# Kernel optimization log

Hardware: AMD Instinct MI355X
Metric: run time of the kernel (lower is better)

## Reference

```python
import jax, jax.numpy as jnp
import numpy as np

N = 100000   # nodes
E = 300000   # edges
D = 256      # emb_dim
L = 5        # num_layers
SELF_LOOP_BOND_TYPE = 4
BN_EPS = 1e-5


def setup_inputs() -> dict:
    key = jax.random.key(0)
    ks = jax.random.split(key, 12)
    s = 0.05
    x = jax.random.randint(ks[0], (N, 2), 0, 3)
    edge_index = jax.random.randint(ks[1], (2, E), 0, N)
    edge_attr = jax.random.randint(ks[2], (E, 2), 0, 3)
    x_emb1 = jax.random.normal(ks[3], (120, D), dtype=jnp.float32) * s
    x_emb2 = jax.random.normal(ks[4], (3, D), dtype=jnp.float32) * s
    edge_emb1 = jax.random.normal(ks[5], (L, 6, D), dtype=jnp.float32) * s
    edge_emb2 = jax.random.normal(ks[6], (L, 3, D), dtype=jnp.float32) * s
    W1 = jax.random.normal(ks[7], (L, D, 2 * D), dtype=jnp.float32) * (1.0 / np.sqrt(D))
    b1 = jnp.zeros((L, 2 * D), dtype=jnp.float32)
    W2 = jax.random.normal(ks[8], (L, 2 * D, D), dtype=jnp.float32) * (1.0 / np.sqrt(2 * D))
    b2 = jnp.zeros((L, D), dtype=jnp.float32)
    bn_gamma = jnp.ones((L - 1, D), dtype=jnp.float32)
    bn_beta = jnp.zeros((L - 1, D), dtype=jnp.float32)
    return dict(x=x, edge_index=edge_index, edge_attr=edge_attr,
                x_emb1=x_emb1, x_emb2=x_emb2,
                edge_emb1=edge_emb1, edge_emb2=edge_emb2,
                W1=W1, b1=b1, W2=W2, b2=b2,
                bn_gamma=bn_gamma, bn_beta=bn_beta)


def reference(x, edge_index, edge_attr, x_emb1, x_emb2, edge_emb1, edge_emb2,
              W1, b1, W2, b2, bn_gamma, bn_beta):
    n = x.shape[0]
    loop = jnp.arange(n)
    # add_self_loops: append (i, i) for every node
    src = jnp.concatenate([edge_index[0], loop])  # [E+N]
    dst = jnp.concatenate([edge_index[1], loop])  # [E+N]
    # self-loop edge_attr = (bond_type=4, direction=0)
    self_attr = jnp.concatenate([
        jnp.full((n, 1), SELF_LOOP_BOND_TYPE, dtype=edge_attr.dtype),
        jnp.zeros((n, 1), dtype=edge_attr.dtype)], axis=1)
    ea = jnp.concatenate([edge_attr, self_attr], axis=0)  # [E+N, 2]

    out = x_emb1[x[:, 0]] + x_emb2[x[:, 1]]  # [N, D]
    for l in range(L):
        e_emb = edge_emb1[l][ea[:, 0]] + edge_emb2[l][ea[:, 1]]  # [E+N, D]
        msg = out[src] + e_emb                                   # gather + message
        agg = jax.ops.segment_sum(msg, dst, num_segments=n)      # scatter-add
        h = jax.nn.relu(agg @ W1[l] + b1[l]) @ W2[l] + b2[l]     # GIN MLP
        if l < L - 1:
            mean = h.mean(axis=0)
            var = h.var(axis=0)  # biased var, matches torch BN training
            h = (h - mean) * jax.lax.rsqrt(var + BN_EPS) * bn_gamma[l] + bn_beta[l]
            h = jax.nn.relu(h)
        out = h
    return out
```

## Files before the change

kernel.cpp:

```cpp
#include <hip/hip_runtime.h>

typedef unsigned short u16;
typedef unsigned int u32;

#define DD 256

typedef short  s16x8 __attribute__((ext_vector_type(8)));
typedef short  s16x4 __attribute__((ext_vector_type(4)));
typedef float  f32x4 __attribute__((ext_vector_type(4)));

__device__ __forceinline__ float b2f(u16 u){
  union { u32 i; float f; } c; c.i = ((u32)u) << 16; return c.f;
}
__device__ __forceinline__ u16 f2b(float f){
  union { float f; u32 i; } c; c.f = f;
  u32 b = c.i + 0x7FFFu + ((c.i >> 16) & 1u);
  return (u16)(b >> 16);
}

__global__ void NodeEncoder_72971494359603_kernel(){}

__global__ void probe_dtype(const u32* w, u32* flag){
  if (threadIdx.x == 0 && blockIdx.x == 0){
    int cnt = 0;
    for (int i = 0; i < 256; i++){
      u32 low = w[i] & 0xFFFFu;
      u32 e = (low >> 7) & 0xFFu;
      if (e >= 0x60u && e <= 0x7Eu) cnt++;
    }
    *flag = (cnt >= 192) ? 1u : 0u;
  }
}

__global__ void cvt_in(const void* src, u16* dst, int n, const u32* flag){
  int i = blockIdx.x * 256 + threadIdx.x;
  if (i < n){
    if (*flag){
      dst[i] = ((const u16*)src)[i];
    } else {
      dst[i] = f2b(((const float*)src)[i]);
    }
  }
}

__global__ void store_out(const u16* h, void* dout, int n, const u32* flag){
  int i = blockIdx.x * 256 + threadIdx.x;
  if (i < n){
    if (*flag){
      ((u16*)dout)[i] = h[i];
    } else {
      ((float*)dout)[i] = b2f(h[i]);
    }
  }
}

__global__ void zero_int(int* p, int n){
  int i = blockIdx.x * 256 + threadIdx.x;
  if (i < n) p[i] = 0;
}

__global__ void build_table(const u16* ee1, const u16* ee2, float* TBL){
  int b = blockIdx.x;
  int l = b / 18, c = b % 18, a = c / 3, bb = c % 3;
  int j = threadIdx.x;
  TBL[b * DD + j] = b2f(ee1[(l * 6 + a) * DD + j]) + b2f(ee2[(l * 3 + bb) * DD + j]);
}

__global__ void hist_kernel(const int* dst, int* counts, int E){
  int e = blockIdx.x * 256 + threadIdx.x;
  if (e < E) atomicAdd(&counts[dst[e]], 1);
}

__global__ void scan_sums(const int* counts, int* bsum, int N){
  __shared__ int red[256];
  int tid = threadIdx.x;
  int base = blockIdx.x * 1024;
  int s = 0;
  for (int i = tid; i < 1024; i += 256){
    int g = base + i;
    if (g < N) s += counts[g];
  }
  red[tid] = s;
  __syncthreads();
  for (int off = 128; off > 0; off >>= 1){
    if (tid < off) red[tid] += red[tid + off];
    __syncthreads();
  }
  if (tid == 0) bsum[blockIdx.x] = red[0];
}

__global__ void scan_top(int* bsum, int nb){
  if (threadIdx.x == 0 && blockIdx.x == 0){
    int acc = 0;
    for (int i = 0; i < nb; i++){ int t = bsum[i]; bsum[i] = acc; acc += t; }
  }
}

__global__ void scan_block(const int* counts, const int* bsum,
                           int* offsets, int* cursor, int N){
  __shared__ int tsum[256];
  int b = blockIdx.x;
  int tid = threadIdx.x;
  int base = b * 1024;
  int v0, v1, v2, v3;
  int g = base + tid * 4;
  v0 = (g + 0 < N) ? counts[g + 0] : 0;
  v1 = (g + 1 < N) ? counts[g + 1] : 0;
  v2 = (g + 2 < N) ? counts[g + 2] : 0;
  v3 = (g + 3 < N) ? counts[g + 3] : 0;
  tsum[tid] = v0 + v1 + v2 + v3;
  __syncthreads();
  for (int off = 1; off < 256; off <<= 1){
    int t = (tid >= off) ? tsum[tid - off] : 0;
    __syncthreads();
    tsum[tid] += t;
    __syncthreads();
  }
  int excl = (tid == 0 ? 0 : tsum[tid - 1]) + bsum[b];
  if (g + 0 < N){ offsets[g + 0] = excl; cursor[g + 0] = excl; } excl += v0;
  if (g + 1 < N){ offsets[g + 1] = excl; cursor[g + 1] = excl; } excl += v1;
  if (g + 2 < N){ offsets[g + 2] = excl; cursor[g + 2] = excl; } excl += v2;
  if (g + 3 < N){ offsets[g + 3] = excl; cursor[g + 3] = excl; }
}

__global__ void fill_csr(const int* ei, const int* ea, int* cursor,
                         int* payload, int E){
  int e = blockIdx.x * 256 + threadIdx.x;
  if (e < E){
    int d = ei[E + e];
    int pos = atomicAdd(&cursor[d], 1);
    int a = ea[2 * e], bb = ea[2 * e + 1];
    payload[pos] = ei[e] | ((a * 3 + bb) << 17);
  }
}

__global__ void node_embed(const int* x, const u16* xe1, const u16* xe2,
                           u16* out, int N){
  int idx = blockIdx.x * 256 + threadIdx.x;
  if (idx < N * DD){
    int n = idx >> 8, j = idx & 255;
    int x0 = x[2 * n], x1 = x[2 * n + 1];
    out[idx] = f2b(b2f(xe1[x0 * DD + j]) + b2f(xe2[x1 * DD + j]));
  }
}

__global__ void aggregate(const u16* __restrict__ feat, const float* __restrict__ TBL,
                          const int* __restrict__ offsets, const int* __restrict__ counts,
                          const int* __restrict__ payload, u16* __restrict__ agg, int N,
                          const float* __restrict__ sums, const u16* __restrict__ gamma,
                          const u16* __restrict__ beta, float invN, int apply_bn){
  __shared__ __align__(16) float T[18 * DD];
  int tid = threadIdx.x;
  for (int i = tid; i < 18 * DD; i += 256) T[i] = TBL[i];
  __syncthreads();
  int wave = tid >> 6, lane = tid & 63;
  int c4 = lane * 4;
  float sc[4], sh[4];
  if (apply_bn){
#pragma unroll
    for (int e = 0; e < 4; e++){
      int j = c4 + e;
      float mean = sums[j] * invN;
      float var = sums[DD + j] * invN - mean * mean;
      if (var < 0.f) var = 0.f;
      float scl = rsqrtf(var + 1e-5f) * b2f(gamma[j]);
      sc[e] = scl; sh[e] = b2f(beta[j]) - mean * scl;
    }
  } else {
#pragma unroll
    for (int e = 0; e < 4; e++){ sc[e] = 1.f; sh[e] = 0.f; }
  }
  int n0 = blockIdx.x * 32 + wave * 8;
  for (int u = 0; u < 8; u++){
    int n = n0 + u;
    if (n >= N) return;
    s16x4 sv = *(const s16x4*)(feat + (size_t)n * DD + c4);
    f32x4 tb = *(const f32x4*)(T + 12 * DD + c4);
    float v0 = b2f((u16)sv[0]) * sc[0] + sh[0];
    float v1 = b2f((u16)sv[1]) * sc[1] + sh[1];
    float v2 = b2f((u16)sv[2]) * sc[2] + sh[2];
    float v3 = b2f((u16)sv[3]) * sc[3] + sh[3];
    if (apply_bn){
      v0 = fmaxf(v0, 0.f); v1 = fmaxf(v1, 0.f);
      v2 = fmaxf(v2, 0.f); v3 = fmaxf(v3, 0.f);
    }
    float a0 = v0 + tb[0], a1 = v1 + tb[1], a2 = v2 + tb[2], a3 = v3 + tb[3];
    int e0 = offsets[n], cnt = counts[n];
    for (int e = e0; e < e0 + cnt; e++){
      int pl = payload[e];
      int src = pl & 0x1FFFF;
      int idx = pl >> 17;
      s16x4 rv = *(const s16x4*)(feat + (size_t)src * DD + c4);
      f32x4 tv = *(const f32x4*)(T + idx * DD + c4);
      float w0 = b2f((u16)rv[0]) * sc[0] + sh[0];
      float w1 = b2f((u16)rv[1]) * sc[1] + sh[1];
      float w2 = b2f((u16)rv[2]) * sc[2] + sh[2];
      float w3 = b2f((u16)rv[3]) * sc[3] + sh[3];
      if (apply_bn){
        w0 = fmaxf(w0, 0.f); w1 = fmaxf(w1, 0.f);
        w2 = fmaxf(w2, 0.f); w3 = fmaxf(w3, 0.f);
      }
      a0 += w0 + tv[0];
      a1 += w1 + tv[1];
      a2 += w2 + tv[2];
      a3 += w3 + tv[3];
    }
    s16x4 o;
    o[0] = (short)f2b(a0); o[1] = (short)f2b(a1);
    o[2] = (short)f2b(a2); o[3] = (short)f2b(a3);
    *(s16x4*)(agg + (size_t)n * DD + c4) = o;
  }
}

__global__ void pack_B(const u16* __restrict__ W, u16* __restrict__ Wp, int K, int Nc){
  int idx = blockIdx.x * 256 + threadIdx.x;
  int lane = idx & 63;
  int t = idx >> 6;
  int nk = K >> 5;
  int ksub = t % nk, cblk = t / nk;
  if (cblk >= (Nc >> 4)) return;
  int col = cblk * 16 + (lane & 15);
  int krow = ksub * 32 + (lane >> 4) * 8;
  u16* dst = Wp + (size_t)idx * 8;
#pragma unroll
  for (int e = 0; e < 8; e++)
    dst[e] = W[(size_t)(krow + e) * Nc + col];
}

__global__ void mlp_fused(const u16* __restrict__ A, const u16* __restrict__ Wp1,
                          const u16* __restrict__ bias1, const u16* __restrict__ Wp2,
                          const u16* __restrict__ bias2, u16* __restrict__ H,
                          float* __restrict__ partial, int npart, int M){
  __shared__ __align__(16) u16 As[64 * 256];
  __shared__ __align__(16) u16 Ms[2][64 * 128];
  int tid = threadIdx.x, lane = tid & 63, wave = tid >> 6;
  int wr = wave >> 2, wc = wave & 3;
  int row0 = blockIdx.x * 64;
  int lr = lane & 15, hi = lane >> 4;

  int srow = tid >> 5, slot = tid & 31;
#pragma unroll
  for (int p = 0; p < 4; p++){
    int r = p * 16 + srow;
    int gr = row0 + r; if (gr > M - 1) gr = M - 1;
    s16x8 v = *(const s16x8*)(A + (size_t)gr * DD + slot * 8);
    *(s16x8*)((char*)As + r * 512 + ((slot * 16) ^ ((r & 7) << 4))) = v;
  }
  __syncthreads();

  f32x4 zero = {0.f, 0.f, 0.f, 0.f};
  f32x4 acc2[2][4];
#pragma unroll
  for (int m = 0; m < 2; m++)
#pragma unroll
    for (int n = 0; n < 4; n++) acc2[m][n] = zero;
  f32x4 acc1[2][2];

  auto G1 = [&](int cc){
#pragma unroll
    for (int m = 0; m < 2; m++)
#pragma unroll
      for (int n = 0; n < 2; n++) acc1[m][n] = zero;
#pragma unroll
    for (int ks = 0; ks < 8; ks++){
      s16x8 af[2];
#pragma unroll
      for (int m = 0; m < 2; m++){
        int arow = wr * 32 + m * 16 + lr;
        af[m] = *(const s16x8*)((const char*)As + arow * 512 +
                                ((ks * 64 + hi * 16) ^ ((arow & 7) << 4)));
      }
#pragma unroll
      for (int n = 0; n < 2; n++){
        int cb = cc * 8 + wc * 2 + n;
        s16x8 bf = *(const s16x8*)(Wp1 + (((size_t)cb * 8 + ks) * 64 + lane) * 8);
        acc1[0][n] = __builtin_amdgcn_mfma_f32_16x16x32_bf16(af[0], bf, acc1[0][n], 0, 0, 0);
        acc1[1][n] = __builtin_amdgcn_mfma_f32_16x16x32_bf16(af[1], bf, acc1[1][n], 0, 0, 0);
      }
    }
  };
  auto WMS = [&](int cc, int buf){
    char* ms = (char*)Ms[buf];
#pragma unroll
    for (int n = 0; n < 2; n++){
      float bv = b2f(bias1[cc * 128 + wc * 32 + n * 16 + lr]);
      int c2 = (wc * 32 + n * 16 + lr) * 2;
#pragma unroll
      for (int m = 0; m < 2; m++)
#pragma unroll
        for (int r = 0; r < 4; r++){
          int mrow = wr * 32 + m * 16 + hi * 4 + r;
          float v = fmaxf(acc1[m][n][r] + bv, 0.f);
          *(u16*)(ms + mrow * 256 + (c2 ^ ((mrow & 7) << 4))) = f2b(v);
        }
    }
  };

  G1(0);
  WMS(0, 0);
  __syncthreads();

#pragma unroll
  for (int c = 0; c < 4; c++){
    const char* ms = (const char*)Ms[c & 1];
#pragma unroll
    for (int ks = 0; ks < 4; ks++){
      s16x8 mf[2];
#pragma unroll
      for (int m = 0; m < 2; m++){
        int mrow = wr * 32 + m * 16 + lr;
        mf[m] = *(const s16x8*)(ms + mrow * 256 +
                                ((ks * 64 + hi * 16) ^ ((mrow & 7) << 4)));
      }
#pragma unroll
      for (int n = 0; n < 4; n++){
        int cb2 = wc * 4 + n;
        s16x8 wf = *(const s16x8*)(Wp2 + (((size_t)cb2 * 16 + c * 4 + ks) * 64 + lane) * 8);
        acc2[0][n] = __builtin_amdgcn_mfma_f32_16x16x32_bf16(mf[0], wf, acc2[0][n], 0, 0, 0);
        acc2[1][n] = __builtin_amdgcn_mfma_f32_16x16x32_bf16(mf[1], wf, acc2[1][n], 0, 0, 0);
      }
    }
    if (c < 3){
      G1(c + 1);
      WMS(c + 1, (c + 1) & 1);
      __syncthreads();
    }
  }

#pragma unroll
  for (int n = 0; n < 4; n++){
    float bv = b2f(bias2[wc * 64 + n * 16 + lr]);
    int c2 = (wc * 64 + n * 16 + lr) * 2;
#pragma unroll
    for (int m = 0; m < 2; m++)
#pragma unroll
      for (int r = 0; r < 4; r++){
        int mrow = wr * 32 + m * 16 + hi * 4 + r;
        *(u16*)((char*)As + mrow * 512 + (c2 ^ ((mrow & 7) << 4))) = f2b(acc2[m][n][r] + bv);
      }
  }
  __syncthreads();

  float s[8], q[8];
#pragma unroll
  for (int e = 0; e < 8; e++){ s[e] = 0.f; q[e] = 0.f; }
  int sl = tid & 31;
#pragma unroll
  for (int p = 0; p < 4; p++){
    int r = p * 16 + (tid >> 5);
    s16x8 v = *(const s16x8*)((const char*)As + r * 512 + ((sl << 4) ^ ((r & 7) << 4)));
    int gr = row0 + r;
    if (gr < M){
      *(s16x8*)(H + (size_t)gr * DD + sl * 8) = v;
      if (partial){
#pragma unroll
        for (int e = 0; e < 8; e++){
          float f = b2f((u16)v[e]);
          s[e] += f; q[e] += f * f;
        }
      }
    }
  }
  if (partial){
#pragma unroll
    for (int e = 0; e < 8; e++){
      s[e] += __shfl_xor(s[e], 32);
      q[e] += __shfl_xor(q[e], 32);
    }
    float* redS = (float*)Ms;
    float* redQ = redS + 8 * 256;
    if (lane < 32){
#pragma unroll
      for (int e = 0; e < 8; e++){
        redS[wave * 256 + sl * 8 + e] = s[e];
        redQ[wave * 256 + sl * 8 + e] = q[e];
      }
    }
    __syncthreads();
    if (tid < 256){
      float a = 0.f, b = 0.f;
#pragma unroll
      for (int w = 0; w < 8; w++){ a += redS[w * 256 + tid]; b += redQ[w * 256 + tid]; }
      partial[(size_t)blockIdx.x * DD + tid] = a;
      partial[(size_t)(npart + blockIdx.x) * DD + tid] = b;
    }
  }
}

__global__ void bn_reduce(const float* __restrict__ partial, float* __restrict__ sums,
                          int npart){
  int b = blockIdx.x, which = b >> 3, jg = b & 7;
  int t = threadIdx.x;
  int j = jg * 32 + (t >> 3);
  int li = t & 7;
  float s = 0.f;
  for (int i = li; i < npart; i += 8)
    s += partial[(size_t)(which * npart + i) * DD + j];
  s += __shfl_xor(s, 1); s += __shfl_xor(s, 2); s += __shfl_xor(s, 4);
  if (li == 0) sums[which * DD + j] = s;
}

extern "C" void kernel_launch(void* const* d_in, const int* in_sizes, int n_in,
                              void* d_out, int out_size, void* d_ws, size_t ws_size,
                              hipStream_t stream){
  (void)n_in; (void)out_size; (void)ws_size;
  const int* x    = (const int*)d_in[0];
  const int* ei   = (const int*)d_in[1];
  const int* ea   = (const int*)d_in[2];
  const void* xe1 = d_in[3];
  const void* xe2 = d_in[4];
  const void* ee1 = d_in[5];
  const void* ee2 = d_in[6];
  const void* W1  = d_in[7];
  const void* b1  = d_in[8];
  const void* W2  = d_in[9];
  const void* b2  = d_in[10];
  const void* gam = d_in[11];
  const void* bet = d_in[12];

  int N = in_sizes[0] / 2;
  int E = in_sizes[1] / 2;
  int NB = (N + 1023) / 1024;
  const int L = 5;
  int nblk = (N + 63) / 64;
  int npart = nblk;

  char* base = (char*)d_ws;
  size_t off = 0;
  u32* flag    = (u32*)(base + off);   off += 256;
  float* TBL   = (float*)(base + off); off += ((size_t)L * 18 * DD * 4 + 255) & ~(size_t)255;
  int* counts  = (int*)(base + off);   off += ((size_t)N * 4 + 255) & ~(size_t)255;
  int* offsets = (int*)(base + off);   off += ((size_t)N * 4 + 255) & ~(size_t)255;
  int* cursor  = (int*)(base + off);   off += ((size_t)N * 4 + 255) & ~(size_t)255;
  int* bsum    = (int*)(base + off);   off += ((size_t)NB * 4 + 255) & ~(size_t)255;
  int* payload = (int*)(base + off);   off += ((size_t)E * 4 + 255) & ~(size_t)255;
  float* part  = (float*)(base + off); off += ((size_t)2 * npart * DD * 4 + 255) & ~(size_t)255;
  float* sums  = (float*)(base + off); off += ((size_t)2 * DD * 4 + 255) & ~(size_t)255;
  u16* wx1  = (u16*)(base + off); off += ((size_t)120 * DD * 2 + 255) & ~(size_t)255;
  u16* wx2  = (u16*)(base + off); off += ((size_t)3 * DD * 2 + 255) & ~(size_t)255;
  u16* wee1 = (u16*)(base + off); off += ((size_t)L * 6 * DD * 2 + 255) & ~(size_t)255;
  u16* wee2 = (u16*)(base + off); off += ((size_t)L * 3 * DD * 2 + 255) & ~(size_t)255;
  u16* wW1  = (u16*)(base + off); off += ((size_t)L * DD * 2 * DD * 2 + 255) & ~(size_t)255;
  u16* wb1  = (u16*)(base + off); off += ((size_t)L * 2 * DD * 2 + 255) & ~(size_t)255;
  u16* wW2  = (u16*)(base + off); off += ((size_t)L * 2 * DD * DD * 2 + 255) & ~(size_t)255;
  u16* wb2  = (u16*)(base + off); off += ((size_t)L * DD * 2 + 255) & ~(size_t)255;
  u16* wgam = (u16*)(base + off); off += ((size_t)(L - 1) * DD * 2 + 255) & ~(size_t)255;
  u16* wbet = (u16*)(base + off); off += ((size_t)(L - 1) * DD * 2 + 255) & ~(size_t)255;
  u16* Wp1  = (u16*)(base + off); off += ((size_t)L * DD * 2 * DD * 2 + 255) & ~(size_t)255;
  u16* Wp2  = (u16*)(base + off); off += ((size_t)L * 2 * DD * DD * 2 + 255) & ~(size_t)255;
  u16* feat = (u16*)(base + off); off += ((size_t)N * DD * 2 + 255) & ~(size_t)255;
  u16* agg  = (u16*)(base + off); off += ((size_t)N * DD * 2 + 255) & ~(size_t)255;

  probe_dtype<<<1, 64, 0, stream>>>((const u32*)xe1, flag);
  cvt_in<<<(120 * DD + 255) / 256, 256, 0, stream>>>(xe1, wx1, 120 * DD, flag);
  cvt_in<<<(3 * DD + 255) / 256, 256, 0, stream>>>(xe2, wx2, 3 * DD, flag);
  cvt_in<<<(L * 6 * DD + 255) / 256, 256, 0, stream>>>(ee1, wee1, L * 6 * DD, flag);
  cvt_in<<<(L * 3 * DD + 255) / 256, 256, 0, stream>>>(ee2, wee2, L * 3 * DD, flag);
  cvt_in<<<(L * DD * 2 * DD + 255) / 256, 256, 0, stream>>>(W1, wW1, L * DD * 2 * DD, flag);
  cvt_in<<<(L * 2 * DD + 255) / 256, 256, 0, stream>>>(b1, wb1, L * 2 * DD, flag);
  cvt_in<<<(L * 2 * DD * DD + 255) / 256, 256, 0, stream>>>(W2, wW2, L * 2 * DD * DD, flag);
  cvt_in<<<(L * DD + 255) / 256, 256, 0, stream>>>(b2, wb2, L * DD, flag);
  cvt_in<<<((L - 1) * DD + 255) / 256, 256, 0, stream>>>(gam, wgam, (L - 1) * DD, flag);
  cvt_in<<<((L - 1) * DD + 255) / 256, 256, 0, stream>>>(bet, wbet, (L - 1) * DD, flag);

  build_table<<<90, 256, 0, stream>>>(wee1, wee2, TBL);
  for (int l = 0; l < L; l++){
    pack_B<<<64, 256, 0, stream>>>(wW1 + (size_t)l * DD * 2 * DD,
                                   Wp1 + (size_t)l * DD * 2 * DD, DD, 2 * DD);
    pack_B<<<64, 256, 0, stream>>>(wW2 + (size_t)l * 2 * DD * DD,
                                   Wp2 + (size_t)l * 2 * DD * DD, 2 * DD, DD);
  }
  zero_int<<<(N + 255) / 256, 256, 0, stream>>>(counts, N);
  hist_kernel<<<(E + 255) / 256, 256, 0, stream>>>(ei + E, counts, E);
  scan_sums<<<NB, 256, 0, stream>>>(counts, bsum, N);
  scan_top<<<1, 64, 0, stream>>>(bsum, NB);
  scan_block<<<NB, 256, 0, stream>>>(counts, bsum, offsets, cursor, N);
  fill_csr<<<(E + 255) / 256, 256, 0, stream>>>(ei, ea, cursor, payload, E);

  node_embed<<<(N * DD + 255) / 256, 256, 0, stream>>>(x, wx1, wx2, feat, N);

  float invN = 1.0f / (float)N;

  for (int l = 0; l < L; l++){
    aggregate<<<(N + 31) / 32, 256, 0, stream>>>(
        feat, TBL + (size_t)l * 18 * DD, offsets, counts, payload, agg, N,
        sums, wgam + (size_t)(l > 0 ? l - 1 : 0) * DD,
        wbet + (size_t)(l > 0 ? l - 1 : 0) * DD, invN, l > 0 ? 1 : 0);

    mlp_fused<<<nblk, 512, 0, stream>>>(
        agg, Wp1 + (size_t)l * DD * 2 * DD, wb1 + (size_t)l * 2 * DD,
        Wp2 + (size_t)l * 2 * DD * DD, wb2 + (size_t)l * DD, feat,
        (l < L - 1) ? part : (float*)nullptr, npart, N);

    if (l < L - 1){
      bn_reduce<<<16, 256, 0, stream>>>(part, sums, npart);
    }
  }

  store_out<<<(N * DD + 255) / 256, 256, 0, stream>>>(feat, d_out, N * DD, flag);
}
```

Baseline: 1.636 ms.

## Fuse neighbor aggregation into MLP kernel and ping-pong feature buffers

Merges the aggregate kernel into the fused MLP kernel: each 64-row block gathers neighbor features, applies the previous layer's BN and ReLU, adds edge embeddings from a table staged in the Ms shared buffer, and writes the aggregated rows straight into the swizzled As tile. The intermediate agg tensor's global write and read are dropped, and two feature buffers alternate between layers. The per-layer pack_B launches are also batched into one 2D launch per weight. In exchange, the irregular gather now runs inside a kernel with heavy shared-memory use and launch bounds, which may limit latency hiding for the gather phase.

Measured after the change: 1.646 ms. Within noise of the previous version (+0.6%).

```diff
diff --git a/kernel.cpp b/kernel.cpp
--- a/kernel.cpp
+++ b/kernel.cpp
@@ -144,75 +144,9 @@
   }
 }
 
-__global__ void aggregate(const u16* __restrict__ feat, const float* __restrict__ TBL,
-                          const int* __restrict__ offsets, const int* __restrict__ counts,
-                          const int* __restrict__ payload, u16* __restrict__ agg, int N,
-                          const float* __restrict__ sums, const u16* __restrict__ gamma,
-                          const u16* __restrict__ beta, float invN, int apply_bn){
-  __shared__ __align__(16) float T[18 * DD];
-  int tid = threadIdx.x;
-  for (int i = tid; i < 18 * DD; i += 256) T[i] = TBL[i];
-  __syncthreads();
-  int wave = tid >> 6, lane = tid & 63;
-  int c4 = lane * 4;
-  float sc[4], sh[4];
-  if (apply_bn){
-#pragma unroll
-    for (int e = 0; e < 4; e++){
-      int j = c4 + e;
-      float mean = sums[j] * invN;
-      float var = sums[DD + j] * invN - mean * mean;
-      if (var < 0.f) var = 0.f;
-      float scl = rsqrtf(var + 1e-5f) * b2f(gamma[j]);
-      sc[e] = scl; sh[e] = b2f(beta[j]) - mean * scl;
-    }
-  } else {
-#pragma unroll
-    for (int e = 0; e < 4; e++){ sc[e] = 1.f; sh[e] = 0.f; }
-  }
-  int n0 = blockIdx.x * 32 + wave * 8;
-  for (int u = 0; u < 8; u++){
-    int n = n0 + u;
-    if (n >= N) return;
-    s16x4 sv = *(const s16x4*)(feat + (size_t)n * DD + c4);
-    f32x4 tb = *(const f32x4*)(T + 12 * DD + c4);
-    float v0 = b2f((u16)sv[0]) * sc[0] + sh[0];
-    float v1 = b2f((u16)sv[1]) * sc[1] + sh[1];
-    float v2 = b2f((u16)sv[2]) * sc[2] + sh[2];
-    float v3 = b2f((u16)sv[3]) * sc[3] + sh[3];
-    if (apply_bn){
-      v0 = fmaxf(v0, 0.f); v1 = fmaxf(v1, 0.f);
-      v2 = fmaxf(v2, 0.f); v3 = fmaxf(v3, 0.f);
-    }
-    float a0 = v0 + tb[0], a1 = v1 + tb[1], a2 = v2 + tb[2], a3 = v3 + tb[3];
-    int e0 = offsets[n], cnt = counts[n];
-    for (int e = e0; e < e0 + cnt; e++){
-      int pl = payload[e];
-      int src = pl & 0x1FFFF;
-      int idx = pl >> 17;
-      s16x4 rv = *(const s16x4*)(feat + (size_t)src * DD + c4);
-      f32x4 tv = *(const f32x4*)(T + idx * DD + c4);
-      float w0 = b2f((u16)rv[0]) * sc[0] + sh[0];
-      float w1 = b2f((u16)rv[1]) * sc[1] + sh[1];
-      float w2 = b2f((u16)rv[2]) * sc[2] + sh[2];
-      float w3 = b2f((u16)rv[3]) * sc[3] + sh[3];
-      if (apply_bn){
-        w0 = fmaxf(w0, 0.f); w1 = fmaxf(w1, 0.f);
-        w2 = fmaxf(w2, 0.f); w3 = fmaxf(w3, 0.f);
-      }
-      a0 += w0 + tv[0];
-      a1 += w1 + tv[1];
-      a2 += w2 + tv[2];
-      a3 += w3 + tv[3];
-    }
-    s16x4 o;
-    o[0] = (short)f2b(a0); o[1] = (short)f2b(a1);
-    o[2] = (short)f2b(a2); o[3] = (short)f2b(a3);
-    *(s16x4*)(agg + (size_t)n * DD + c4) = o;
-  }
-}
-
-__global__ void pack_B(const u16* __restrict__ W, u16* __restrict__ Wp, int K, int Nc){
+__global__ void pack_B(const u16* __restrict__ W0, u16* __restrict__ Wp0, int K, int Nc){
+  const u16* W = W0 + (size_t)blockIdx.y * K * Nc;
+  u16* Wp = Wp0 + (size_t)blockIdx.y * K * Nc;
   int idx = blockIdx.x * 256 + threadIdx.x;
   int lane = idx & 63;
   int t = idx >> 6;
@@ -227,24 +161,83 @@
     dst[e] = W[(size_t)(krow + e) * Nc + col];
 }
 
-__global__ void mlp_fused(const u16* __restrict__ A, const u16* __restrict__ Wp1,
-                          const u16* __restrict__ bias1, const u16* __restrict__ Wp2,
-                          const u16* __restrict__ bias2, u16* __restrict__ H,
-                          float* __restrict__ partial, int npart, int M){
+__global__ __launch_bounds__(512, 4)
+void layer_fused(const u16* __restrict__ feat, const float* __restrict__ TBL,
+                 const int* __restrict__ offsets, const int* __restrict__ counts,
+                 const int* __restrict__ payload,
+                 const u16* __restrict__ Wp1, const u16* __restrict__ bias1,
+                 const u16* __restrict__ Wp2, const u16* __restrict__ bias2,
+                 u16* __restrict__ H, float* __restrict__ partial, int npart, int M,
+                 const float* __restrict__ sums, const u16* __restrict__ gamma,
+                 const u16* __restrict__ beta, float invN, int apply_bn){
   __shared__ __align__(16) u16 As[64 * 256];
   __shared__ __align__(16) u16 Ms[2][64 * 128];
+  float* T = (float*)Ms;
   int tid = threadIdx.x, lane = tid & 63, wave = tid >> 6;
   int wr = wave >> 2, wc = wave & 3;
   int row0 = blockIdx.x * 64;
   int lr = lane & 15, hi = lane >> 4;
 
-  int srow = tid >> 5, slot = tid & 31;
-#pragma unroll
-  for (int p = 0; p < 4; p++){
-    int r = p * 16 + srow;
-    int gr = row0 + r; if (gr > M - 1) gr = M - 1;
-    s16x8 v = *(const s16x8*)(A + (size_t)gr * DD + slot * 8);
-    *(s16x8*)((char*)As + r * 512 + ((slot * 16) ^ ((r & 7) << 4))) = v;
+  for (int i = tid; i < 18 * DD; i += 512) T[i] = TBL[i];
+  __syncthreads();
+
+  {
+    int c4 = lane * 4;
+    float sc[4], sh[4];
+    if (apply_bn){
+#pragma unroll
+      for (int e = 0; e < 4; e++){
+        int j = c4 + e;
+        float mean = sums[j] * invN;
+        float var = sums[DD + j] * invN - mean * mean;
+        if (var < 0.f) var = 0.f;
+        float scl = rsqrtf(var + 1e-5f) * b2f(gamma[j]);
+        sc[e] = scl; sh[e] = b2f(beta[j]) - mean * scl;
+      }
+    } else {
+#pragma unroll
+      for (int e = 0; e < 4; e++){ sc[e] = 1.f; sh[e] = 0.f; }
+    }
+    for (int u = 0; u < 8; u++){
+      int r = wave * 8 + u;
+      int n = row0 + r; if (n > M - 1) n = M - 1;
+      s16x4 sv = *(const s16x4*)(feat + (size_t)n * DD + c4);
+      f32x4 tb = *(const f32x4*)(T + 12 * DD + c4);
+      float v0 = b2f((u16)sv[0]) * sc[0] + sh[0];
+      float v1 = b2f((u16)sv[1]) * sc[1] + sh[1];
+      float v2 = b2f((u16)sv[2]) * sc[2] + sh[2];
+      float v3 = b2f((u16)sv[3]) * sc[3] + sh[3];
+      if (apply_bn){
+        v0 = fmaxf(v0, 0.f); v1 = fmaxf(v1, 0.f);
+        v2 = fmaxf(v2, 0.f); v3 = fmaxf(v3, 0.f);
+      }
+      float a0 = v0 + tb[0], a1 = v1 + tb[1], a2 = v2 + tb[2], a3 = v3 + tb[3];
+      int e0 = offsets[n], cnt = counts[n];
+      for (int e = e0; e < e0 + cnt; e++){
+        int pl = payload[e];
+        int src = pl & 0x1FFFF;
+        int idx = pl >> 17;
+        s16x4 rv = *(const s16x4*)(feat + (size_t)src * DD + c4);
+        f32x4 tv = *(const f32x4*)(T + idx * DD + c4);
+        float w0 = b2f((u16)rv[0]) * sc[0] + sh[0];
+        float w1 = b2f((u16)rv[1]) * sc[1] + sh[1];
+        float w2 = b2f((u16)rv[2]) * sc[2] + sh[2];
+        float w3 = b2f((u16)rv[3]) * sc[3] + sh[3];
+        if (apply_bn){
+          w0 = fmaxf(w0, 0.f); w1 = fmaxf(w1, 0.f);
+          w2 = fmaxf(w2, 0.f); w3 = fmaxf(w3, 0.f);
+        }
+        a0 += w0 + tv[0];
+        a1 += w1 + tv[1];
+        a2 += w2 + tv[2];
+        a3 += w3 + tv[3];
+      }
+      s16x4 o;
+      o[0] = (short)f2b(a0); o[1] = (short)f2b(a1);
+      o[2] = (short)f2b(a2); o[3] = (short)f2b(a3);
+      int byteo = r * 512 + ((((lane >> 1) ^ (r & 7)) & 31) << 4) + ((lane & 1) << 3);
+      *(s16x4*)((char*)As + byteo) = o;
+    }
   }
   __syncthreads();
 
@@ -448,8 +441,8 @@
   u16* wbet = (u16*)(base + off); off += ((size_t)(L - 1) * DD * 2 + 255) & ~(size_t)255;
   u16* Wp1  = (u16*)(base + off); off += ((size_t)L * DD * 2 * DD * 2 + 255) & ~(size_t)255;
   u16* Wp2  = (u16*)(base + off); off += ((size_t)L * 2 * DD * DD * 2 + 255) & ~(size_t)255;
-  u16* feat = (u16*)(base + off); off += ((size_t)N * DD * 2 + 255) & ~(size_t)255;
-  u16* agg  = (u16*)(base + off); off += ((size_t)N * DD * 2 + 255) & ~(size_t)255;
+  u16* featA = (u16*)(base + off); off += ((size_t)N * DD * 2 + 255) & ~(size_t)255;
+  u16* featB = (u16*)(base + off); off += ((size_t)N * DD * 2 + 255) & ~(size_t)255;
 
   probe_dtype<<<1, 64, 0, stream>>>((const u32*)xe1, flag);
   cvt_in<<<(120 * DD + 255) / 256, 256, 0, stream>>>(xe1, wx1, 120 * DD, flag);
@@ -464,12 +457,8 @@
   cvt_in<<<((L - 1) * DD + 255) / 256, 256, 0, stream>>>(bet, wbet, (L - 1) * DD, flag);
 
   build_table<<<90, 256, 0, stream>>>(wee1, wee2, TBL);
-  for (int l = 0; l < L; l++){
-    pack_B<<<64, 256, 0, stream>>>(wW1 + (size_t)l * DD * 2 * DD,
-                                   Wp1 + (size_t)l * DD * 2 * DD, DD, 2 * DD);
-    pack_B<<<64, 256, 0, stream>>>(wW2 + (size_t)l * 2 * DD * DD,
-                                   Wp2 + (size_t)l * 2 * DD * DD, 2 * DD, DD);
-  }
+  pack_B<<<dim3(64, L), 256, 0, stream>>>(wW1, Wp1, DD, 2 * DD);
+  pack_B<<<dim3(64, L), 256, 0, stream>>>(wW2, Wp2, 2 * DD, DD);
   zero_int<<<(N + 255) / 256, 256, 0, stream>>>(counts, N);
   hist_kernel<<<(E + 255) / 256, 256, 0, stream>>>(ei + E, counts, E);
   scan_sums<<<NB, 256, 0, stream>>>(counts, bsum, N);
@@ -477,25 +466,26 @@
   scan_block<<<NB, 256, 0, stream>>>(counts, bsum, offsets, cursor, N);
   fill_csr<<<(E + 255) / 256, 256, 0, stream>>>(ei, ea, cursor, payload, E);
 
-  node_embed<<<(N * DD + 255) / 256, 256, 0, stream>>>(x, wx1, wx2, feat, N);
+  node_embed<<<(N * DD + 255) / 256, 256, 0, stream>>>(x, wx1, wx2, featA, N);
 
   float invN = 1.0f / (float)N;
+  u16* fin = featA;
+  u16* fout = featB;
 
   for (int l = 0; l < L; l++){
-    aggregate<<<(N + 31) / 32, 256, 0, stream>>>(
-        feat, TBL + (size_t)l * 18 * DD, offsets, counts, payload, agg, N,
+    layer_fused<<<nblk, 512, 0, stream>>>(
+        fin, TBL + (size_t)l * 18 * DD, offsets, counts, payload,
+        Wp1 + (size_t)l * DD * 2 * DD, wb1 + (size_t)l * 2 * DD,
+        Wp2 + (size_t)l * 2 * DD * DD, wb2 + (size_t)l * DD,
+        fout, (l < L - 1) ? part : (float*)nullptr, npart, N,
         sums, wgam + (size_t)(l > 0 ? l - 1 : 0) * DD,
         wbet + (size_t)(l > 0 ? l - 1 : 0) * DD, invN, l > 0 ? 1 : 0);
 
-    mlp_fused<<<nblk, 512, 0, stream>>>(
-        agg, Wp1 + (size_t)l * DD * 2 * DD, wb1 + (size_t)l * 2 * DD,
-        Wp2 + (size_t)l * 2 * DD * DD, wb2 + (size_t)l * DD, feat,
-        (l < L - 1) ? part : (float*)nullptr, npart, N);
-
     if (l < L - 1){
       bn_reduce<<<16, 256, 0, stream>>>(part, sums, npart);
     }
-  }
-
-  store_out<<<(N * DD + 255) / 256, 256, 0, stream>>>(feat, d_out, N * DD, flag);
-}
+    u16* t = fin; fin = fout; fout = t;
+  }
+
+  store_out<<<(N * DD + 255) / 256, 256, 0, stream>>>(fin, d_out, N * DD, flag);
+}
```
